# Kernel tuning notes

Measured on AMD Instinct MI355X. Metric: run time of the kernel, lower is better.

## Reference

```python
import jax, jax.numpy as jnp
import numpy as np

DIMS = [2048, 1024, 512, 256, 128, 64, 32, 16, 8, 4, 2]
IN_CH = [3, 8, 32, 64, 64, 64, 128, 256, 512, 512, 512]
FEAT = [8, 32, 64, 64, 64, 128, 256, 512, 512, 512, 1024]
B = 512
K = 16


def setup_inputs() -> dict:
    key = jax.random.key(0)
    keys = jax.random.split(key, 64)
    inp = {"x": jax.random.normal(keys[0], (B, 3, 2048), dtype=jnp.float32)}
    for i, d in enumerate(DIMS):
        inp[f"c{i}"] = jax.random.randint(keys[1 + i], (d,), 0, 3, dtype=jnp.int64)
    for i in range(11):
        cin, f = IN_CH[i], FEAT[i]
        inp[f"W{i+1}"] = jax.random.normal(keys[20 + 2 * i], (3 * f, cin), dtype=jnp.float32) / jnp.sqrt(jnp.float32(cin))
        inp[f"b{i+1}"] = jnp.zeros((3 * f,), dtype=jnp.float32)
    inp["Wfc"] = jax.random.normal(keys[60], (K, 1024), dtype=jnp.float32) / jnp.sqrt(jnp.float32(1024))
    inp["bfc"] = jnp.zeros((K,), dtype=jnp.float32)
    return inp


def _kdconv(x, W, b, sel, featdim, dim):
    # pointwise conv (kernel size 1) + relu: [B, in, dim] -> [B, 3*featdim, dim]
    y = jax.nn.relu(jnp.einsum('oi,bid->bod', W, x) + b[None, :, None])
    bsz = y.shape[0]
    # faithful to torch: view [B, featdim, 3*dim], then gather index d*3 + sel[d]
    y = y.reshape(bsz, featdim, 3 * dim)
    idx = sel + 3 * jnp.arange(dim, dtype=sel.dtype)
    y = jnp.take(y, idx, axis=2)                       # [B, featdim, dim]
    y = y.reshape(bsz, featdim, dim // 2, 2)
    return jnp.max(y, axis=-1)                          # [B, featdim, dim//2]


def reference(x, c0, c1, c2, c3, c4, c5, c6, c7, c8, c9, c10,
              W1, b1, W2, b2, W3, b3, W4, b4, W5, b5, W6, b6,
              W7, b7, W8, b8, W9, b9, W10, b10, W11, b11, Wfc, bfc):
    cs = [c0, c1, c2, c3, c4, c5, c6, c7, c8, c9, c10]
    Ws = [W1, W2, W3, W4, W5, W6, W7, W8, W9, W10, W11]
    bs = [b1, b2, b3, b4, b5, b6, b7, b8, b9, b10, b11]
    y = x
    for i in range(11):
        y = _kdconv(y, Ws[i], bs[i], cs[i], FEAT[i], DIMS[i])
    y = y.reshape(-1, 1024)
    logits = y @ Wfc.T + bfc
    return jax.nn.log_softmax(logits, axis=1)
```

## Files before the change

### kernel.cpp

```cpp
#include <hip/hip_runtime.h>
#include <cstdint>
#include <cmath>


typedef __attribute__((ext_vector_type(8))) short bhalf8;
typedef __attribute__((ext_vector_type(4))) float floatx4;

__device__ __forceinline__ unsigned short f2bf(float f) {
    uint32_t u = __float_as_uint(f);
    u += 0x7FFFu + ((u >> 16) & 1u);
    return (unsigned short)(u >> 16);
}
__device__ __forceinline__ float bf2f(unsigned short u) {
    return __uint_as_float(((uint32_t)u) << 16);
}

struct WPrep {
    const float* src[9];
    unsigned short* dst[9];
    int n4[9];
};

__global__ __launch_bounds__(256)
void l01_kernel(const float* __restrict__ x,
                const float* __restrict__ W0, const float* __restrict__ b0,
                const int* __restrict__ sel0,
                const float* __restrict__ W1, const float* __restrict__ b1,
                const int* __restrict__ sel1,
                unsigned short* __restrict__ out,
                WPrep wp, int nL1) {
    const int tid = threadIdx.x;

    if ((int)blockIdx.x >= nL1) {
        const int stride = (gridDim.x - nL1) * 256;
        const int g0 = (blockIdx.x - nL1) * 256 + tid;
        #pragma unroll
        for (int l = 0; l < 5; ++l) {
            const float4* s = reinterpret_cast<const float4*>(wp.src[l]);
            uint2* d = reinterpret_cast<uint2*>(wp.dst[l]);
            for (int i = g0; i < wp.n4[l]; i += stride) {
                const float4 v = s[i];
                uint2 o;
                o.x = (uint32_t)f2bf(v.x) | ((uint32_t)f2bf(v.y) << 16);
                o.y = (uint32_t)f2bf(v.z) | ((uint32_t)f2bf(v.w) << 16);
                d[i] = o;
            }
        }
        return;
    }

    __shared__ float W0s[24][3]; __shared__ float b0s[24];
    __shared__ float W1s[96][8]; __shared__ float b1s[96];
    if (tid < 24) {
        W0s[tid][0] = W0[tid * 3 + 0];
        W0s[tid][1] = W0[tid * 3 + 1];
        W0s[tid][2] = W0[tid * 3 + 2];
        b0s[tid] = b0[tid];
    }
    if (tid < 96) {
        #pragma unroll
        for (int k = 0; k < 8; ++k) W1s[tid][k] = W1[tid * 8 + k];
        b1s[tid] = b1[tid];
    }
    __syncthreads();

    const int gid = blockIdx.x * 256 + tid;
    const int b  = gid >> 9;
    const int j1 = gid & 511;
    const float* xb = x + (size_t)b * 3 * 2048;

    float cols[2][8];
    int q1v[2];
    #pragma unroll
    for (int pos1 = 0; pos1 < 2; ++pos1) {
        const int d1 = 2 * j1 + pos1;
        const int e1 = 3 * d1 + sel1[d1];
        const int q1 = (e1 >= 1024) + (e1 >= 2048);
        const int p1 = e1 - q1 * 1024;
        q1v[pos1] = q1;

        float xv[2][3]; int qq0[2];
        #pragma unroll
        for (int pos0 = 0; pos0 < 2; ++pos0) {
            const int d0 = 2 * p1 + pos0;
            const int e0 = 3 * d0 + sel0[d0];
            const int q0 = (e0 >= 2048) + (e0 >= 4096);
            const int p0 = e0 - q0 * 2048;
            qq0[pos0] = q0;
            xv[pos0][0] = xb[p0];
            xv[pos0][1] = xb[2048 + p0];
            xv[pos0][2] = xb[4096 + p0];
        }
        #pragma unroll
        for (int f = 0; f < 8; ++f) {
            const int r0 = 3 * f + qq0[0], r1 = 3 * f + qq0[1];
            const float v0 = b0s[r0] + W0s[r0][0]*xv[0][0] + W0s[r0][1]*xv[0][1] + W0s[r0][2]*xv[0][2];
            const float v1 = b0s[r1] + W0s[r1][0]*xv[1][0] + W0s[r1][1]*xv[1][1] + W0s[r1][2]*xv[1][2];
            cols[pos1][f] = fmaxf(fmaxf(v0, v1), 0.f);
        }
    }

    unsigned short o[32];
    #pragma unroll
    for (int f = 0; f < 32; ++f) {
        const int r0 = 3 * f + q1v[0], r1 = 3 * f + q1v[1];
        float v0 = b1s[r0], v1 = b1s[r1];
        #pragma unroll
        for (int k = 0; k < 8; ++k) {
            v0 = fmaf(cols[0][k], W1s[r0][k], v0);
            v1 = fmaf(cols[1][k], W1s[r1][k], v1);
        }
        o[f] = f2bf(fmaxf(fmaxf(v0, v1), 0.f));
    }
    bhalf8* op = reinterpret_cast<bhalf8*>(out + (size_t)gid * 32);
    #pragma unroll
    for (int i = 0; i < 4; ++i) {
        bhalf8 v;
        #pragma unroll
        for (int k = 0; k < 8; ++k) v[k] = (short)o[8*i + k];
        op[i] = v;
    }
}


template<int RB>
__device__ __forceinline__ int swaddr(int row, int colbyte) {
    constexpr int SM = (RB / 16 >= 8) ? 7 : (RB / 16 - 1);
    return row * RB + (colbyte ^ ((row & SM) << 4));
}

template<int DIM, int CIN, int FEAT>
__device__ __forceinline__ void kdlayer(char* pool, int offIn, int offOut,
                                        int offW, int offMisc,
                                        const float* __restrict__ Wg,
                                        const float* __restrict__ bg,
                                        const int* __restrict__ sel, int tid) {
    constexpr int NH  = CIN / 32;
    constexpr int MT  = DIM / 16;
    constexpr int NT  = FEAT / 16;
    constexpr int RBW = CIN * 2;
    constexpr int RBO = FEAT * 2;
    float* biasS = (float*)(pool + offMisc);
    unsigned short* qp = (unsigned short*)(pool + offMisc + 3 * FEAT * 4);

    {
        constexpr int NW4 = 3 * FEAT * CIN / 4;
        const float4* Ws = (const float4*)Wg;
        for (int i = tid; i < NW4; i += 256) {
            const float4 v = Ws[i];
            const int row = (i * 4) / CIN, col = (i * 4) % CIN;
            uint2 o;
            o.x = (uint32_t)f2bf(v.x) | ((uint32_t)f2bf(v.y) << 16);
            o.y = (uint32_t)f2bf(v.z) | ((uint32_t)f2bf(v.w) << 16);
            *(uint2*)(pool + offW + swaddr<RBW>(row, col * 2)) = o;
        }
    }
    for (int i = tid; i < 3 * FEAT; i += 256) biasS[i] = bg[i];
    for (int d = tid; d < DIM; d += 256) {
        const int e = 3 * d + sel[d];
        const int q = (e >= DIM) + (e >= 2 * DIM);
        qp[d] = (unsigned short)((q << 12) | (e - q * DIM));
    }
    __syncthreads();

    const int lane = tid & 63, wave = tid >> 6;
    const int g = lane >> 4, l15 = lane & 15;
    for (int mt = wave; mt < MT; mt += 4) {
        const int pa = qp[mt * 16 + l15] & 0xFFF;
        bhalf8 aF[NH];
        #pragma unroll
        for (int ks = 0; ks < NH; ++ks)
            aF[ks] = *(const bhalf8*)(pool + offIn +
                        swaddr<RBW>(pa, (ks * 32 + g * 8) * 2));
        const int r0 = mt * 16 + g * 4;
        int qv[4];
        #pragma unroll
        for (int i = 0; i < 4; ++i) qv[i] = qp[r0 + i] >> 12;
        const int j0 = mt * 8 + g * 2;
        #pragma unroll
        for (int nt = 0; nt < NT; ++nt) {
            const int f = nt * 16 + l15;
            floatx4 acc[3];
            #pragma unroll
            for (int q = 0; q < 3; ++q) acc[q] = (floatx4){0.f, 0.f, 0.f, 0.f};
            #pragma unroll
            for (int q = 0; q < 3; ++q)
                #pragma unroll
                for (int ks = 0; ks < NH; ++ks) {
                    const bhalf8 bF = *(const bhalf8*)(pool + offW +
                        swaddr<RBW>(3 * f + q, (ks * 32 + g * 8) * 2));
                    acc[q] = __builtin_amdgcn_mfma_f32_16x16x32_bf16(
                        aF[ks], bF, acc[q], 0, 0, 0);
                }
            float v[4];
            #pragma unroll
            for (int i = 0; i < 4; ++i) {
                const float a0 = acc[0][i], a1 = acc[1][i], a2 = acc[2][i];
                const int qi = qv[i];
                const float pre = (qi == 0) ? a0 : (qi == 1 ? a1 : a2);
                v[i] = pre + biasS[3 * f + qi];
            }
            *(unsigned short*)(pool + offOut + swaddr<RBO>(j0, f * 2)) =
                f2bf(fmaxf(fmaxf(v[0], v[1]), 0.f));
            *(unsigned short*)(pool + offOut + swaddr<RBO>(j0 + 1, f * 2)) =
                f2bf(fmaxf(fmaxf(v[2], v[3]), 0.f));
        }
    }
    __syncthreads();
}

__global__ __launch_bounds__(256)
void chain_kernel(const unsigned short* __restrict__ act,
                  unsigned short* __restrict__ out,
                  const float* __restrict__ W2, const float* __restrict__ b2, const int* __restrict__ s2,
                  const float* __restrict__ W3, const float* __restrict__ b3, const int* __restrict__ s3,
                  const float* __restrict__ W4, const float* __restrict__ b4, const int* __restrict__ s4,
                  const float* __restrict__ W5, const float* __restrict__ b5, const int* __restrict__ s5) {
    __shared__ __align__(16) char pool[79872];
    const int tid = threadIdx.x;
    const int b = blockIdx.x;

    {
        const char* src = (const char*)(act + (size_t)b * 512 * 32);
        #pragma unroll
        for (int k = 0; k < 8; ++k) {
            const int off = tid * 16 + k * 4096;
            const bhalf8 v = *(const bhalf8*)(src + off);
            *(bhalf8*)(pool + swaddr<64>(off >> 6, off & 63)) = v;
        }
    }

    kdlayer<512, 32,  64>(pool, 0,     47104, 32768, 45056, W2, b2, s2, tid);
    kdlayer<256, 64,  64>(pool, 47104, 0,     16384, 40960, W3, b3, s3, tid);
    kdlayer<128, 64,  64>(pool, 0,     16384, 24576, 49152, W4, b4, s4, tid);
    kdlayer< 64, 64, 128>(pool, 16384, 0,     24576, 73728, W5, b5, s5, tid);

    {
        char* dst = (char*)(out + (size_t)b * 32 * 128);
        #pragma unroll
        for (int k = 0; k < 2; ++k) {
            const int off = tid * 16 + k * 4096;
            const bhalf8 v = *(const bhalf8*)(pool + swaddr<256>(off >> 8, off & 255));
            *(bhalf8*)(dst + off) = v;
        }
    }
}

template<int CIN, int BT>
__global__ __launch_bounds__(256)
void kdmfma_kernel(const unsigned short* __restrict__ act,
                   const unsigned short* __restrict__ Wq,
                   const float* __restrict__ bias,
                   const int*   __restrict__ sel,
                   unsigned short* __restrict__ out,
                   int feat, int dim, int nbt) {
    constexpr int KS  = (CIN >= 128) ? 128 : CIN;
    constexpr int NH  = KS / 32;
    constexpr int LDK = KS + 8;
    constexpr int TPA = 256 / BT;
    constexpr int EA  = KS / TPA;
    constexpr int NSA = EA / 8;
    constexpr int NSW = KS / 32;
    constexpr int MF  = 2;
    constexpr int NF  = (BT == 64) ? 2 : 1;
    __shared__ __align__(16) unsigned short Ab[BT][LDK];
    __shared__ __align__(16) unsigned short Wb[64][LDK];

    const int dimh = dim >> 1;
    const int bt = blockIdx.x % nbt;
    const int j  = blockIdx.x / nbt;
    const int f0 = blockIdx.y * 64;
    const int b0 = bt * BT;

    const int tid  = threadIdx.x;
    const int lane = tid & 63;
    const int wave = tid >> 6;

    const int srowA = tid / TPA;
    const int kgA   = (tid % TPA) * EA;
    const int srowW = tid >> 2;
    const int kgW   = (tid & 3) * (KS / 4);

    const int rowBase = (BT == 64) ? (wave & 1) * 32 : 0;
    const int colBase = (BT == 64) ? (wave >> 1) * 32 : wave * 16;

    floatx4 acc[2][MF][NF];
    #pragma unroll
    for (int pp = 0; pp < 2; ++pp)
        #pragma unroll
        for (int mi = 0; mi < MF; ++mi)
            #pragma unroll
            for (int ni = 0; ni < NF; ++ni)
                acc[pp][mi][ni] = (floatx4){0.f, 0.f, 0.f, 0.f};
    int qv[2];

    #pragma unroll
    for (int pp = 0; pp < 2; ++pp) {
        const int d = 2 * j + pp;
        const int s = sel[d];
        const int e = 3 * d + s;
        const int q = (e >= dim) + (e >= 2 * dim);
        const int p = e - q * dim;
        qv[pp] = q;

        const unsigned short* Ap = act + ((size_t)(b0 + srowA) * dim + p) * CIN + kgA;
        const unsigned short* Wp = Wq + ((size_t)(3 * (f0 + srowW) + q)) * CIN + kgW;

        bhalf8 pa[NSA], pw[NSW];
        #pragma unroll
        for (int u = 0; u < NSA; ++u)
            pa[u] = *reinterpret_cast<const bhalf8*>(Ap + u * 8);
        #pragma unroll
        for (int u = 0; u < NSW; ++u)
            pw[u] = *reinterpret_cast<const bhalf8*>(Wp + u * 8);

        for (int k0 = 0; k0 < CIN; k0 += KS) {
            __syncthreads();
            #pragma unroll
            for (int u = 0; u < NSA; ++u)
                *reinterpret_cast<bhalf8*>(&Ab[srowA][kgA + u * 8]) = pa[u];
            #pragma unroll
            for (int u = 0; u < NSW; ++u)
                *reinterpret_cast<bhalf8*>(&Wb[srowW][kgW + u * 8]) = pw[u];
            if (k0 + KS < CIN) {
                #pragma unroll
                for (int u = 0; u < NSA; ++u)
                    pa[u] = *reinterpret_cast<const bhalf8*>(Ap + k0 + KS + u * 8);
                #pragma unroll
                for (int u = 0; u < NSW; ++u)
                    pw[u] = *reinterpret_cast<const bhalf8*>(Wp + k0 + KS + u * 8);
            }
            __syncthreads();

            #pragma unroll
            for (int ks = 0; ks < NH; ++ks) {
                const int kk = ks * 32 + (lane >> 4) * 8;
                bhalf8 aF[MF], bF[NF];
                #pragma unroll
                for (int mi = 0; mi < MF; ++mi)
                    aF[mi] = *reinterpret_cast<const bhalf8*>(
                        &Ab[rowBase + mi * 16 + (lane & 15)][kk]);
                #pragma unroll
                for (int ni = 0; ni < NF; ++ni)
                    bF[ni] = *reinterpret_cast<const bhalf8*>(
                        &Wb[colBase + ni * 16 + (lane & 15)][kk]);
                #pragma unroll
                for (int mi = 0; mi < MF; ++mi)
                    #pragma unroll
                    for (int ni = 0; ni < NF; ++ni)
                        acc[pp][mi][ni] = __builtin_amdgcn_mfma_f32_16x16x32_bf16(
                            aF[mi], bF[ni], acc[pp][mi][ni], 0, 0, 0);
            }
        }
    }

    const int orow = (lane >> 4) << 2;
    const int ocol = lane & 15;
    #pragma unroll
    for (int mi = 0; mi < MF; ++mi)
        #pragma unroll
        for (int ni = 0; ni < NF; ++ni) {
            const int fc = f0 + colBase + ni * 16 + ocol;
            const float bv0 = bias[3 * fc + qv[0]];
            const float bv1 = bias[3 * fc + qv[1]];
            #pragma unroll
            for (int i = 0; i < 4; ++i) {
                const int br = b0 + rowBase + mi * 16 + orow + i;
                const float v = fmaxf(fmaxf(acc[0][mi][ni][i] + bv0,
                                            acc[1][mi][ni][i] + bv1), 0.f);
                out[((size_t)br * dimh + j) * feat + fc] = f2bf(v);
            }
        }
}

__global__ __launch_bounds__(256)
void fc_lsm_kernel(const unsigned short* __restrict__ y,
                   const float* __restrict__ Wfc,
                   const float* __restrict__ bfc,
                   float* __restrict__ out) {
    const int b   = blockIdx.x;
    const int tid = threadIdx.x;
    __shared__ __align__(16) float ys[1024];
    __shared__ float lg[16];

    {
        const ushort4 v = reinterpret_cast<const ushort4*>(y + (size_t)b * 1024)[tid];
        ys[tid * 4 + 0] = bf2f(v.x);
        ys[tid * 4 + 1] = bf2f(v.y);
        ys[tid * 4 + 2] = bf2f(v.z);
        ys[tid * 4 + 3] = bf2f(v.w);
    }
    __syncthreads();

    const int l = tid >> 4, lane = tid & 15;
    const float4* w4 = reinterpret_cast<const float4*>(Wfc + (size_t)l * 1024);
    const float4* y4 = reinterpret_cast<const float4*>(ys);
    float p = 0.f;
    #pragma unroll
    for (int i = 0; i < 16; ++i) {
        const float4 a = y4[lane + 16 * i];
        const float4 w = w4[lane + 16 * i];
        p += a.x * w.x + a.y * w.y + a.z * w.z + a.w * w.w;
    }
    #pragma unroll
    for (int off = 8; off > 0; off >>= 1) p += __shfl_down(p, off, 16);
    if (lane == 0) lg[l] = p + bfc[l];
    __syncthreads();

    if (tid < 16) {
        float m = -1e30f;
        #pragma unroll
        for (int i = 0; i < 16; ++i) m = fmaxf(m, lg[i]);
        float s = 0.f;
        #pragma unroll
        for (int i = 0; i < 16; ++i) s += expf(lg[i] - m);
        out[b * 16 + tid] = lg[tid] - m - logf(s);
    }
}

extern "C" void kernel_launch(void* const* d_in, const int* in_sizes, int n_in,
                              void* d_out, int out_size, void* d_ws, size_t ws_size,
                              hipStream_t stream) {
    static const int LFEAT[11] = {8, 32, 64, 64, 64, 128, 256, 512, 512, 512, 1024};
    static const int LDIM[11]  = {2048, 1024, 512, 256, 128, 64, 32, 16, 8, 4, 2};
    static const int LCIN[11]  = {3, 8, 32, 64, 64, 64, 128, 256, 512, 512, 512};

    const float* x = (const float*)d_in[0];
    const int B = in_sizes[0] / (3 * 2048);

    const size_t slot = (size_t)B * 32 * 512;
    float* bufA = (float*)d_ws;
    float* bufB = bufA + slot;
    unsigned short* wq = (unsigned short*)(bufB + slot);

    const float* W[11]; const float* bi[11]; const int* sl[11];
    for (int i = 0; i < 11; ++i) {
        W[i]  = (const float*)d_in[12 + 2 * i];
        bi[i] = (const float*)d_in[13 + 2 * i];
        sl[i] = (const int*)d_in[1 + i];
    }

    unsigned short* wqp[11];
    {
        size_t off = 0;
        for (int i = 6; i <= 10; ++i) {
            wqp[i] = wq + off;
            off += (size_t)3 * LFEAT[i] * LCIN[i];
        }
    }

    unsigned short* actA = (unsigned short*)bufA;
    unsigned short* actB = (unsigned short*)bufB;

    {
        WPrep wp;
        for (int i = 6; i <= 10; ++i) {
            wp.src[i - 6] = W[i];
            wp.dst[i - 6] = wqp[i];
            wp.n4[i - 6]  = (3 * LFEAT[i] * LCIN[i]) / 4;
        }
        for (int l = 5; l < 9; ++l) { wp.src[l] = nullptr; wp.dst[l] = nullptr; wp.n4[l] = 0; }
        const int nL1 = (B * 512) / 256;
        l01_kernel<<<nL1 + 768, 256, 0, stream>>>(x, W[0], bi[0], sl[0],
                                                  W[1], bi[1], sl[1],
                                                  actB, wp, nL1);
    }

    chain_kernel<<<B, 256, 0, stream>>>(actB, actA,
                                        W[2], bi[2], sl[2],
                                        W[3], bi[3], sl[3],
                                        W[4], bi[4], sl[4],
                                        W[5], bi[5], sl[5]);

    const int nbt64 = B / 64;
    const int nbt32 = B / 32;

    {   dim3 g((LDIM[6]/2) * nbt64, LFEAT[6]/64);
        kdmfma_kernel<128, 64><<<g, 256, 0, stream>>>(actA, wqp[6], bi[6], sl[6], actB, LFEAT[6], LDIM[6], nbt64); }
    {   dim3 g((LDIM[7]/2) * nbt64, LFEAT[7]/64);
        kdmfma_kernel<256, 64><<<g, 256, 0, stream>>>(actB, wqp[7], bi[7], sl[7], actA, LFEAT[7], LDIM[7], nbt64); }

    {   dim3 g((LDIM[8]/2) * nbt32, LFEAT[8]/64);
        kdmfma_kernel<512, 32><<<g, 256, 0, stream>>>(actA, wqp[8], bi[8], sl[8], actB, LFEAT[8], LDIM[8], nbt32); }
    {   dim3 g((LDIM[9]/2) * nbt32, LFEAT[9]/64);
        kdmfma_kernel<512, 32><<<g, 256, 0, stream>>>(actB, wqp[9], bi[9], sl[9], actA, LFEAT[9], LDIM[9], nbt32); }
    {   dim3 g((LDIM[10]/2) * nbt32, LFEAT[10]/64);
        kdmfma_kernel<512, 32><<<g, 256, 0, stream>>>(actA, wqp[10], bi[10], sl[10], actB, LFEAT[10], LDIM[10], nbt32); }

    fc_lsm_kernel<<<B, 256, 0, stream>>>(actB, (const float*)d_in[34],
                                         (const float*)d_in[35], (float*)d_out);
}
```

Baseline: 102.3 us.

## Pre-swizzle chain weights to bf16 once and widen chain kernel to 512 threads

The weights for layers 2-5 are now converted to bf16 once, in the prep blocks of the first kernel, and written already swizzled. Each chain-kernel block then does a plain 16-byte copy into shared memory instead of converting floats itself for every batch element. The chain kernel moves to 512 threads with a 2D wave tiling: A fragments are kept in registers, and B fragments are loaded once per N tile and reused across the M tiles. The first kernel also writes its output pre-swizzled so the chain kernel can load it with straight copies. The costs are higher register pressure from holding fragments, a larger prep workload in the first kernel, and possibly lower occupancy at 512 threads.

```diff
diff --git a/kernel.cpp b/kernel.cpp
--- a/kernel.cpp
+++ b/kernel.cpp
@@ -19,6 +19,8 @@
     const float* src[9];
     unsigned short* dst[9];
     int n4[9];
+    int csh[4];
+    int sm[4];
 };
 
 __global__ __launch_bounds__(256)
@@ -35,7 +37,26 @@
         const int stride = (gridDim.x - nL1) * 256;
         const int g0 = (blockIdx.x - nL1) * 256 + tid;
         #pragma unroll
-        for (int l = 0; l < 5; ++l) {
+        for (int l = 0; l < 4; ++l) {
+            const float4* s = reinterpret_cast<const float4*>(wp.src[l]);
+            char* dbase = (char*)wp.dst[l];
+            const int n16 = wp.n4[l] >> 1;
+            const int csh = wp.csh[l], sm = wp.sm[l];
+            for (int i = g0; i < n16; i += stride) {
+                const float4 va = s[2 * i], vb = s[2 * i + 1];
+                uint4 o;
+                o.x = (uint32_t)f2bf(va.x) | ((uint32_t)f2bf(va.y) << 16);
+                o.y = (uint32_t)f2bf(va.z) | ((uint32_t)f2bf(va.w) << 16);
+                o.z = (uint32_t)f2bf(vb.x) | ((uint32_t)f2bf(vb.y) << 16);
+                o.w = (uint32_t)f2bf(vb.z) | ((uint32_t)f2bf(vb.w) << 16);
+                const int row = i >> csh;
+                const int c   = i - (row << csh);
+                *(uint4*)(dbase + (row << (csh + 4)) +
+                          ((c * 16) ^ ((row & sm) << 4))) = o;
+            }
+        }
+        #pragma unroll
+        for (int l = 4; l < 9; ++l) {
             const float4* s = reinterpret_cast<const float4*>(wp.src[l]);
             uint2* d = reinterpret_cast<uint2*>(wp.dst[l]);
             for (int i = g0; i < wp.n4[l]; i += stride) {
@@ -113,12 +134,13 @@
         o[f] = f2bf(fmaxf(fmaxf(v0, v1), 0.f));
     }
     bhalf8* op = reinterpret_cast<bhalf8*>(out + (size_t)gid * 32);
+    const int perm = j1 & 3;
     #pragma unroll
     for (int i = 0; i < 4; ++i) {
         bhalf8 v;
         #pragma unroll
         for (int k = 0; k < 8; ++k) v[k] = (short)o[8*i + k];
-        op[i] = v;
+        op[i ^ perm] = v;
     }
 }
 
@@ -132,7 +154,7 @@
 template<int DIM, int CIN, int FEAT>
 __device__ __forceinline__ void kdlayer(char* pool, int offIn, int offOut,
                                         int offW, int offMisc,
-                                        const float* __restrict__ Wg,
+                                        const unsigned short* __restrict__ Wq,
                                         const float* __restrict__ bg,
                                         const int* __restrict__ sel, int tid) {
     constexpr int NH  = CIN / 32;
@@ -140,67 +162,79 @@
     constexpr int NT  = FEAT / 16;
     constexpr int RBW = CIN * 2;
     constexpr int RBO = FEAT * 2;
+    constexpr int WM  = (MT < 8) ? MT : 8;
+    constexpr int WN  = 8 / WM;
+    constexpr int MPW = MT / WM;
+    constexpr int NPW = NT / WN;
+    constexpr int WG16 = 3 * FEAT * CIN / 8;
+
     float* biasS = (float*)(pool + offMisc);
     unsigned short* qp = (unsigned short*)(pool + offMisc + 3 * FEAT * 4);
 
     {
-        constexpr int NW4 = 3 * FEAT * CIN / 4;
-        const float4* Ws = (const float4*)Wg;
-        for (int i = tid; i < NW4; i += 256) {
-            const float4 v = Ws[i];
-            const int row = (i * 4) / CIN, col = (i * 4) % CIN;
-            uint2 o;
-            o.x = (uint32_t)f2bf(v.x) | ((uint32_t)f2bf(v.y) << 16);
-            o.y = (uint32_t)f2bf(v.z) | ((uint32_t)f2bf(v.w) << 16);
-            *(uint2*)(pool + offW + swaddr<RBW>(row, col * 2)) = o;
-        }
-    }
-    for (int i = tid; i < 3 * FEAT; i += 256) biasS[i] = bg[i];
-    for (int d = tid; d < DIM; d += 256) {
+        const bhalf8* src = (const bhalf8*)Wq;
+        bhalf8* dst = (bhalf8*)(pool + offW);
+        for (int i = tid; i < WG16; i += 512) dst[i] = src[i];
+    }
+    for (int i = tid; i < 3 * FEAT; i += 512) biasS[i] = bg[i];
+    for (int d = tid; d < DIM; d += 512) {
         const int e = 3 * d + sel[d];
         const int q = (e >= DIM) + (e >= 2 * DIM);
         qp[d] = (unsigned short)((q << 12) | (e - q * DIM));
     }
     __syncthreads();
 
-    const int lane = tid & 63, wave = tid >> 6;
-    const int g = lane >> 4, l15 = lane & 15;
-    for (int mt = wave; mt < MT; mt += 4) {
+    const int wv = tid >> 6, ln = tid & 63;
+    const int g = ln >> 4, l15 = ln & 15;
+    const int wm = wv % WM, wn = wv / WM;
+
+    bhalf8 aC[MPW][NH];
+    uint32_t qpk[MPW];
+    #pragma unroll
+    for (int i = 0; i < MPW; ++i) {
+        const int mt = wm + i * WM;
         const int pa = qp[mt * 16 + l15] & 0xFFF;
-        bhalf8 aF[NH];
         #pragma unroll
         for (int ks = 0; ks < NH; ++ks)
-            aF[ks] = *(const bhalf8*)(pool + offIn +
-                        swaddr<RBW>(pa, (ks * 32 + g * 8) * 2));
-        const int r0 = mt * 16 + g * 4;
-        int qv[4];
-        #pragma unroll
-        for (int i = 0; i < 4; ++i) qv[i] = qp[r0 + i] >> 12;
-        const int j0 = mt * 8 + g * 2;
-        #pragma unroll
-        for (int nt = 0; nt < NT; ++nt) {
-            const int f = nt * 16 + l15;
-            floatx4 acc[3];
-            #pragma unroll
-            for (int q = 0; q < 3; ++q) acc[q] = (floatx4){0.f, 0.f, 0.f, 0.f};
-            #pragma unroll
-            for (int q = 0; q < 3; ++q)
-                #pragma unroll
-                for (int ks = 0; ks < NH; ++ks) {
-                    const bhalf8 bF = *(const bhalf8*)(pool + offW +
-                        swaddr<RBW>(3 * f + q, (ks * 32 + g * 8) * 2));
-                    acc[q] = __builtin_amdgcn_mfma_f32_16x16x32_bf16(
-                        aF[ks], bF, acc[q], 0, 0, 0);
-                }
+            aC[i][ks] = *(const bhalf8*)(pool + offIn +
+                          swaddr<RBW>(pa, (ks * 32 + g * 8) * 2));
+        const ushort4 qq = *(const ushort4*)(qp + mt * 16 + g * 4);
+        qpk[i] = (uint32_t)(qq.x >> 12) | ((uint32_t)(qq.y >> 12) << 4)
+               | ((uint32_t)(qq.z >> 12) << 8) | ((uint32_t)(qq.w >> 12) << 12);
+    }
+
+    #pragma unroll
+    for (int ntj = 0; ntj < NPW; ++ntj) {
+        const int nt = wn * NPW + ntj;
+        const int f = nt * 16 + l15;
+        bhalf8 bF[3][NH];
+        #pragma unroll
+        for (int q = 0; q < 3; ++q)
+            #pragma unroll
+            for (int ks = 0; ks < NH; ++ks)
+                bF[q][ks] = *(const bhalf8*)(pool + offW +
+                              swaddr<RBW>(3 * f + q, (ks * 32 + g * 8) * 2));
+        #pragma unroll
+        for (int i = 0; i < MPW; ++i) {
+            floatx4 a0 = (floatx4){0.f,0.f,0.f,0.f};
+            floatx4 a1 = (floatx4){0.f,0.f,0.f,0.f};
+            floatx4 a2 = (floatx4){0.f,0.f,0.f,0.f};
+            #pragma unroll
+            for (int ks = 0; ks < NH; ++ks) {
+                a0 = __builtin_amdgcn_mfma_f32_16x16x32_bf16(aC[i][ks], bF[0][ks], a0, 0, 0, 0);
+                a1 = __builtin_amdgcn_mfma_f32_16x16x32_bf16(aC[i][ks], bF[1][ks], a1, 0, 0, 0);
+                a2 = __builtin_amdgcn_mfma_f32_16x16x32_bf16(aC[i][ks], bF[2][ks], a2, 0, 0, 0);
+            }
+            const int mt = wm + i * WM;
+            const int j0 = mt * 8 + g * 2;
             float v[4];
             #pragma unroll
-            for (int i = 0; i < 4; ++i) {
-                const float a0 = acc[0][i], a1 = acc[1][i], a2 = acc[2][i];
-                const int qi = qv[i];
-                const float pre = (qi == 0) ? a0 : (qi == 1 ? a1 : a2);
-                v[i] = pre + biasS[3 * f + qi];
-            }
-            *(unsigned short*)(pool + offOut + swaddr<RBO>(j0, f * 2)) =
+            for (int r = 0; r < 4; ++r) {
+                const int qi = (qpk[i] >> (4 * r)) & 0xF;
+                const float pre = (qi == 0) ? a0[r] : (qi == 1 ? a1[r] : a2[r]);
+                v[r] = pre + biasS[3 * f + qi];
+            }
+            *(unsigned short*)(pool + offOut + swaddr<RBO>(j0,     f * 2)) =
                 f2bf(fmaxf(fmaxf(v[0], v[1]), 0.f));
             *(unsigned short*)(pool + offOut + swaddr<RBO>(j0 + 1, f * 2)) =
                 f2bf(fmaxf(fmaxf(v[2], v[3]), 0.f));
@@ -209,40 +243,34 @@
     __syncthreads();
 }
 
-__global__ __launch_bounds__(256)
+__global__ __launch_bounds__(512)
 void chain_kernel(const unsigned short* __restrict__ act,
                   unsigned short* __restrict__ out,
-                  const float* __restrict__ W2, const float* __restrict__ b2, const int* __restrict__ s2,
-                  const float* __restrict__ W3, const float* __restrict__ b3, const int* __restrict__ s3,
-                  const float* __restrict__ W4, const float* __restrict__ b4, const int* __restrict__ s4,
-                  const float* __restrict__ W5, const float* __restrict__ b5, const int* __restrict__ s5) {
+                  const unsigned short* __restrict__ w2, const float* __restrict__ b2, const int* __restrict__ s2,
+                  const unsigned short* __restrict__ w3, const float* __restrict__ b3, const int* __restrict__ s3,
+                  const unsigned short* __restrict__ w4, const float* __restrict__ b4, const int* __restrict__ s4,
+                  const unsigned short* __restrict__ w5, const float* __restrict__ b5, const int* __restrict__ s5) {
     __shared__ __align__(16) char pool[79872];
     const int tid = threadIdx.x;
     const int b = blockIdx.x;
 
     {
-        const char* src = (const char*)(act + (size_t)b * 512 * 32);
-        #pragma unroll
-        for (int k = 0; k < 8; ++k) {
-            const int off = tid * 16 + k * 4096;
-            const bhalf8 v = *(const bhalf8*)(src + off);
-            *(bhalf8*)(pool + swaddr<64>(off >> 6, off & 63)) = v;
-        }
-    }
-
-    kdlayer<512, 32,  64>(pool, 0,     47104, 32768, 45056, W2, b2, s2, tid);
-    kdlayer<256, 64,  64>(pool, 47104, 0,     16384, 40960, W3, b3, s3, tid);
-    kdlayer<128, 64,  64>(pool, 0,     16384, 24576, 49152, W4, b4, s4, tid);
-    kdlayer< 64, 64, 128>(pool, 16384, 0,     24576, 73728, W5, b5, s5, tid);
+        const bhalf8* src = (const bhalf8*)(act + (size_t)b * 512 * 32);
+        bhalf8* dst = (bhalf8*)pool;
+        #pragma unroll
+        for (int k = 0; k < 4; ++k) dst[k * 512 + tid] = src[k * 512 + tid];
+    }
+
+    kdlayer<512, 32,  64>(pool, 0,     47104, 32768, 45056, w2, b2, s2, tid);
+    kdlayer<256, 64,  64>(pool, 47104, 0,     16384, 40960, w3, b3, s3, tid);
+    kdlayer<128, 64,  64>(pool, 0,     16384, 24576, 49152, w4, b4, s4, tid);
+    kdlayer< 64, 64, 128>(pool, 16384, 0,     24576, 73728, w5, b5, s5, tid);
 
     {
         char* dst = (char*)(out + (size_t)b * 32 * 128);
-        #pragma unroll
-        for (int k = 0; k < 2; ++k) {
-            const int off = tid * 16 + k * 4096;
-            const bhalf8 v = *(const bhalf8*)(pool + swaddr<256>(off >> 8, off & 255));
-            *(bhalf8*)(dst + off) = v;
-        }
+        const int off = tid * 16;
+        const bhalf8 v = *(const bhalf8*)(pool + swaddr<256>(off >> 8, off & 255));
+        *(bhalf8*)(dst + off) = v;
     }
 }
 
@@ -443,7 +471,7 @@
     unsigned short* wqp[11];
     {
         size_t off = 0;
-        for (int i = 6; i <= 10; ++i) {
+        for (int i = 2; i <= 10; ++i) {
             wqp[i] = wq + off;
             off += (size_t)3 * LFEAT[i] * LCIN[i];
         }
@@ -454,23 +482,25 @@
 
     {
         WPrep wp;
-        for (int i = 6; i <= 10; ++i) {
-            wp.src[i - 6] = W[i];
-            wp.dst[i - 6] = wqp[i];
-            wp.n4[i - 6]  = (3 * LFEAT[i] * LCIN[i]) / 4;
-        }
-        for (int l = 5; l < 9; ++l) { wp.src[l] = nullptr; wp.dst[l] = nullptr; wp.n4[l] = 0; }
+        for (int i = 2; i <= 10; ++i) {
+            wp.src[i - 2] = W[i];
+            wp.dst[i - 2] = wqp[i];
+            wp.n4[i - 2]  = (3 * LFEAT[i] * LCIN[i]) / 4;
+        }
+        static const int CSH[4] = {2, 3, 3, 3};
+        static const int SMV[4] = {3, 7, 7, 7};
+        for (int l = 0; l < 4; ++l) { wp.csh[l] = CSH[l]; wp.sm[l] = SMV[l]; }
         const int nL1 = (B * 512) / 256;
         l01_kernel<<<nL1 + 768, 256, 0, stream>>>(x, W[0], bi[0], sl[0],
                                                   W[1], bi[1], sl[1],
                                                   actB, wp, nL1);
     }
 
-    chain_kernel<<<B, 256, 0, stream>>>(actB, actA,
-                                        W[2], bi[2], sl[2],
-                                        W[3], bi[3], sl[3],
-                                        W[4], bi[4], sl[4],
-                                        W[5], bi[5], sl[5]);
+    chain_kernel<<<B, 512, 0, stream>>>(actB, actA,
+                                        wqp[2], bi[2], sl[2],
+                                        wqp[3], bi[3], sl[3],
+                                        wqp[4], bi[4], sl[4],
+                                        wqp[5], bi[5], sl[5]);
 
     const int nbt64 = B / 64;
     const int nbt32 = B / 32;
```

After: 102.5 us. Within noise of the previous version (+0.2%).
